# Optimization experiments

Hardware: AMD Instinct MI355X
Metric: run time of the kernel (lower is better)

Reference implementation:

```python
import jax, jax.numpy as jnp
import numpy as np

B, S, D = 4, 2048, 1024
H, DK = 16, 64
DOUT = 1024

def setup_inputs() -> dict:
    key = jax.random.key(0)
    ks = jax.random.split(key, 9)
    sc_in = 1.0 / np.sqrt(D)
    sc_cat = 1.0 / np.sqrt(H * DK)
    x = jax.random.normal(ks[0], (B, S, D), dtype=jnp.float32)
    Wq = jax.random.uniform(ks[1], (H, D, DK), jnp.float32, -sc_in, sc_in)
    bq = jax.random.uniform(ks[2], (H, DK), jnp.float32, -sc_in, sc_in)
    Wk = jax.random.uniform(ks[3], (H, D, DK), jnp.float32, -sc_in, sc_in)
    bk = jax.random.uniform(ks[4], (H, DK), jnp.float32, -sc_in, sc_in)
    Wv = jax.random.uniform(ks[5], (H, D, DK), jnp.float32, -sc_in, sc_in)
    bv = jax.random.uniform(ks[6], (H, DK), jnp.float32, -sc_in, sc_in)
    Wo = jax.random.uniform(ks[7], (H * DK, DOUT), jnp.float32, -sc_cat, sc_cat)
    bo = jax.random.uniform(ks[8], (DOUT,), jnp.float32, -sc_cat, sc_cat)
    return {"x": x, "Wq": Wq, "bq": bq, "Wk": Wk, "bk": bk, "Wv": Wv, "bv": bv, "Wo": Wo, "bo": bo}

def reference(x, Wq, bq, Wk, bk, Wv, bv, Wo, bo):
    # Per-head linear projections batched over heads: [B,S,D] x [H,D,K] -> [B,H,S,K]
    Q = jnp.einsum('bsd,hdk->bhsk', x, Wq) + bq[None, :, None, :]
    K = jnp.einsum('bsd,hdk->bhsk', x, Wk) + bk[None, :, None, :]
    V = jnp.einsum('bsd,hdk->bhsk', x, Wv) + bv[None, :, None, :]
    scale = 1.0 / jnp.sqrt(jnp.asarray(DK, dtype=x.dtype))
    scores = jnp.einsum('bhsk,bhtk->bhst', Q, K) * scale  # [B,H,S,S]
    attn = jax.nn.softmax(scores, axis=-1)
    heads = jnp.einsum('bhst,bhtk->bhsk', attn, V)  # [B,H,S,K]
    # concat heads along feature dim (head order = concat order)
    cat = jnp.transpose(heads, (0, 2, 1, 3)).reshape(x.shape[0], x.shape[1], H * DK)
    return cat @ Wo + bo
```

## Files before the change

### kernel.cpp

```cpp
#include <hip/hip_runtime.h>
#include <hip/hip_bf16.h>
#include <stdint.h>

typedef unsigned short u16;
typedef __attribute__((ext_vector_type(8))) short short8;
typedef __attribute__((ext_vector_type(4))) float f32x4;
typedef __attribute__((ext_vector_type(4))) unsigned short u16x4;

#define DEV static __device__ __forceinline__


DEV u16 f2bf(float f) {
  __hip_bfloat16 b = __float2bfloat16(f);
  return *(u16*)&b;
}

DEV void stage16(const u16* g, u16* l) {
  __builtin_amdgcn_global_load_lds((const __attribute__((address_space(1))) void*)g,
                                   (__attribute__((address_space(3))) void*)l, 16, 0, 0);
}

__global__ __launch_bounds__(256) void cvt_kernel(
    const float* __restrict__ x, const float* __restrict__ Wq,
    const float* __restrict__ Wk, const float* __restrict__ Wv,
    const float* __restrict__ Wo,
    u16* __restrict__ xb, u16* __restrict__ Wt, u16* __restrict__ Wot)
{
  int idx = blockIdx.x * 256 + threadIdx.x;
  if (idx < 1048576) {
    int i = idx * 8;
    f32x4 v0 = *(const f32x4*)&x[i];
    f32x4 v1 = *(const f32x4*)&x[i + 4];
    short8 o;
    o[0]=f2bf(v0[0]); o[1]=f2bf(v0[1]); o[2]=f2bf(v0[2]); o[3]=f2bf(v0[3]);
    o[4]=f2bf(v1[0]); o[5]=f2bf(v1[1]); o[6]=f2bf(v1[2]); o[7]=f2bf(v1[3]);
    *(short8*)&xb[i] = o;
  } else if (idx < 1835008) {
    int t = (idx - 1048576) * 4;
    int w = t >> 20; int r = t & 1048575; int n = r >> 10; int d0 = r & 1023;
    const float* W = (w == 0) ? Wq : (w == 1) ? Wk : Wv;
    int h = n >> 6, k = n & 63;
    u16x4 o;
    #pragma unroll
    for (int u = 0; u < 4; u++) o[u] = f2bf(W[(size_t)(h*1024 + d0 + u)*64 + k]);
    *(u16x4*)&Wt[t] = o;
  } else if (idx < 2097152) {
    int t = (idx - 1835008) * 4;
    int n = t >> 10, d0 = t & 1023;
    u16x4 o;
    #pragma unroll
    for (int u = 0; u < 4; u++) o[u] = f2bf(Wo[(size_t)(d0 + u)*1024 + n]);
    *(u16x4*)&Wot[t] = o;
  }
}

DEV void gemm_mainloop(const u16* __restrict__ A, const u16* __restrict__ Bt,
                       int m0, int n0, u16* As, u16* Bs, f32x4 acc[4][4])
{
  const int tid = threadIdx.x;
  const int lane = tid & 63, wid = tid >> 6;
  const int wr = wid >> 1, wc = wid & 1;
  const int qr = lane & 15, g = lane >> 4;
  const int c0 = wid * 2, rA = lane >> 2, cA = (lane & 3) * 8;

  #pragma unroll
  for (int i = 0; i < 4; i++)
    #pragma unroll
    for (int j = 0; j < 4; j++) acc[i][j] = (f32x4){0.f, 0.f, 0.f, 0.f};

  for (int kt = 0; kt < 1024; kt += 32) {
    #pragma unroll
    for (int q = 0; q < 2; q++) {
      const int c = c0 + q;
      stage16(A  + (size_t)(m0 + c*16 + rA)*1024 + kt + cA, &As[c*512]);
      stage16(Bt + (size_t)(n0 + c*16 + rA)*1024 + kt + cA, &Bs[c*512]);
    }
    __syncthreads();
    short8 af[4], bfr[4];
    #pragma unroll
    for (int i = 0; i < 4; i++) af[i]  = *(const short8*)&As[(wr*64 + i*16 + qr)*32 + g*8];
    #pragma unroll
    for (int j = 0; j < 4; j++) bfr[j] = *(const short8*)&Bs[(wc*64 + j*16 + qr)*32 + g*8];
    #pragma unroll
    for (int i = 0; i < 4; i++)
      #pragma unroll
      for (int j = 0; j < 4; j++)
        acc[i][j] = __builtin_amdgcn_mfma_f32_16x16x32_bf16(af[i], bfr[j], acc[i][j], 0, 0, 0);
    __syncthreads();
  }
}

__global__ __launch_bounds__(256) void qkv_gemm_kernel(
    const u16* __restrict__ A, const u16* __restrict__ WtAll,
    const float* __restrict__ bq, const float* __restrict__ bk, const float* __restrict__ bv,
    u16* __restrict__ Qo, u16* __restrict__ Ko, u16* __restrict__ Vo)
{
  __shared__ __align__(128) u16 As[4096];
  __shared__ __align__(128) u16 Bs[4096];
  const int lane = threadIdx.x & 63, wid = threadIdx.x >> 6;
  const int wr = wid >> 1, wc = wid & 1;
  const int qr = lane & 15, g = lane >> 4;
  const int wg = (blockIdx.x & 7) * 192 + (blockIdx.x >> 3);
  const int n0 = (wg & 7) * 128;
  const int m0 = ((wg >> 3) & 63) * 128;
  const int mode = wg >> 9;
  const u16* Bt = WtAll + (size_t)mode * 1048576;
  const float* bias = (mode == 0) ? bq : (mode == 1) ? bk : bv;
  const float osc = (mode == 0) ? 0.1803368867f : 1.0f;

  f32x4 acc[4][4];
  gemm_mainloop(A, Bt, m0, n0, As, Bs, acc);

  if (mode == 2) {
    #pragma unroll
    for (int i = 0; i < 4; i++) {
      const int mrow = m0 + wr*64 + i*16 + g*4;
      const int b = mrow >> 11, s = mrow & 2047;
      #pragma unroll
      for (int j = 0; j < 4; j++) {
        const int n = n0 + wc*64 + j*16 + qr;
        const float bz = bias[n];
        u16x4 v;
        #pragma unroll
        for (int r = 0; r < 4; r++) v[r] = f2bf(acc[i][j][r] + bz);
        *(u16x4*)&Vo[((size_t)(b*16 + (n >> 6))*64 + (n & 63))*2048 + s] = v;
      }
    }
  } else {
    u16* O = (mode == 0) ? Qo : Ko;
    #pragma unroll
    for (int i = 0; i < 4; i++) {
      const int mrow = m0 + wr*64 + i*16 + g*4;
      const int b = mrow >> 11, s = mrow & 2047;
      #pragma unroll
      for (int j = 0; j < 4; j++) {
        const int n = n0 + wc*64 + j*16 + qr;
        const float bz = bias[n];
        const size_t base = ((size_t)(b*16 + (n >> 6))*2048 + s)*64 + (n & 63);
        #pragma unroll
        for (int r = 0; r < 4; r++) O[base + (size_t)r*64] = f2bf((acc[i][j][r] + bz) * osc);
      }
    }
  }
}

__global__ __launch_bounds__(512, 2) void attn_kernel(
    const u16* __restrict__ Q, const u16* __restrict__ K,
    const u16* __restrict__ Vt, u16* __restrict__ cat)
{
  __shared__ __align__(16) u16 Ks[3][2048];
  __shared__ __align__(16) u16 Vs[3][2048];
  __shared__ __align__(16) u16 Pl[10240];
  const int lane = threadIdx.x & 63, w = threadIdx.x >> 6;
  const int bid = blockIdx.x;
  const int logical = (bid & 7) * 32 + (bid >> 3);
  const int bh = logical >> 2;
  const int xq = logical & 3;
  const int b = bh >> 4, h = bh & 15;
  const int q0 = xq * 512 + w * 64;
  const int qr = lane & 15, g = lane >> 4;
  u16* P0 = &Pl[(w*2 + 0)*640];
  u16* P1 = &Pl[(w*2 + 1)*640];

  const u16* Qb = Q  + (size_t)bh * 131072;
  const u16* Kb = K  + (size_t)bh * 131072;
  const u16* Vb = Vt + (size_t)bh * 131072;

  const int isK = (w < 4);
  const int krow = 8*w + (lane >> 3);
  const size_t ksrc = (size_t)krow*64 + (size_t)(((lane & 7) ^ (lane >> 3)) * 8);
  const int vw = w - 4, vrow = 16*vw + (lane >> 2);
  const size_t vsrc = (size_t)vrow*2048 + (size_t)(((lane & 3) ^ ((lane >> 3) & 3)) * 8);
  const int koff = w*512, voff = vw*512;

  const int kro0 = qr*64        + ((g     ^ (qr & 7)) * 8);
  const int kro1 = qr*64        + (((4+g) ^ (qr & 7)) * 8);
  const int kro2 = (16+qr)*64   + ((g     ^ (qr & 7)) * 8);
  const int kro3 = (16+qr)*64   + (((4+g) ^ (qr & 7)) * 8);
  const int vro  = qr*32        + ((g ^ ((qr >> 1) & 3)) * 8);

  short8 qa[4], qb_[4];
  #pragma unroll
  for (int qs = 0; qs < 4; qs++) {
    qa[qs]  = *(const short8*)&Qb[(size_t)(q0 + qs*16 + qr)*64 + g*8];
    qb_[qs] = *(const short8*)&Qb[(size_t)(q0 + qs*16 + qr)*64 + 32 + g*8];
  }

  const short ONE = (short)0x3F80;
  const short8 ones = {ONE, ONE, ONE, ONE, ONE, ONE, ONE, ONE};

  f32x4 o[4][4];
  #pragma unroll
  for (int qs = 0; qs < 4; qs++)
    #pragma unroll
    for (int d = 0; d < 4; d++) o[qs][d] = (f32x4){0.f,0.f,0.f,0.f};
  f32x4 ol[4] = {{0.f,0.f,0.f,0.f},{0.f,0.f,0.f,0.f},{0.f,0.f,0.f,0.f},{0.f,0.f,0.f,0.f}};

  if (isK) {
    stage16(Kb + ksrc,            &Ks[0][koff]);
    stage16(Kb + 2048 + ksrc,     &Ks[1][koff]);
  } else {
    stage16(Vb + vsrc,            &Vs[0][voff]);
    stage16(Vb + vsrc + 32,       &Vs[1][voff]);
  }

  const u16 *kc_cur = &Ks[0][0], *kc_nx1 = &Ks[1][0], *kc_stg = &Ks[2][0];
  const u16 *vc_cur = &Vs[0][0], *vc_nx1 = &Vs[1][0], *vc_stg = &Vs[2][0];

  for (int tt = 0; tt < 2048; tt += 32) {
    asm volatile("s_waitcnt vmcnt(1)" ::: "memory");
    __builtin_amdgcn_s_barrier();
    const int tn = (tt + 64) & 2047;
    if (isK) stage16(Kb + (size_t)tn*64 + ksrc, (u16*)kc_stg + koff);
    else     stage16(Vb + vsrc + tn,            (u16*)vc_stg + voff);

    short8 kc0 = *(const short8*)&kc_cur[kro0];
    short8 kc1 = *(const short8*)&kc_cur[kro1];
    short8 kc2 = *(const short8*)&kc_cur[kro2];
    short8 kc3 = *(const short8*)&kc_cur[kro3];
    short8 vv0 = *(const short8*)&vc_cur[0*512 + vro];
    short8 vv1 = *(const short8*)&vc_cur[1*512 + vro];
    short8 vv2 = *(const short8*)&vc_cur[2*512 + vro];
    short8 vv3 = *(const short8*)&vc_cur[3*512 + vro];

    #pragma unroll
    for (int qs = 0; qs < 4; qs++) {
      f32x4 sl = {0.f,0.f,0.f,0.f}, sh = {0.f,0.f,0.f,0.f};
      sl = __builtin_amdgcn_mfma_f32_16x16x32_bf16(kc0, qa[qs],  sl, 0, 0, 0);
      sl = __builtin_amdgcn_mfma_f32_16x16x32_bf16(kc1, qb_[qs], sl, 0, 0, 0);
      sh = __builtin_amdgcn_mfma_f32_16x16x32_bf16(kc2, qa[qs],  sh, 0, 0, 0);
      sh = __builtin_amdgcn_mfma_f32_16x16x32_bf16(kc3, qb_[qs], sh, 0, 0, 0);
      u16x4 lo, hi;
      #pragma unroll
      for (int r = 0; r < 4; r++) {
        lo[r] = f2bf(__builtin_amdgcn_exp2f(sl[r]));
        hi[r] = f2bf(__builtin_amdgcn_exp2f(sh[r]));
      }
      u16* P = (qs & 1) ? P1 : P0;
      *(u16x4*)&P[qr*40 + g*4]      = lo;
      *(u16x4*)&P[qr*40 + 16 + g*4] = hi;
      short8 bp = *(const short8*)&P[qr*40 + g*8];
      ol[qs] = __builtin_amdgcn_mfma_f32_16x16x32_bf16(ones, bp, ol[qs], 0, 0, 0);
      o[qs][0] = __builtin_amdgcn_mfma_f32_16x16x32_bf16(vv0, bp, o[qs][0], 0, 0, 0);
      o[qs][1] = __builtin_amdgcn_mfma_f32_16x16x32_bf16(vv1, bp, o[qs][1], 0, 0, 0);
      o[qs][2] = __builtin_amdgcn_mfma_f32_16x16x32_bf16(vv2, bp, o[qs][2], 0, 0, 0);
      o[qs][3] = __builtin_amdgcn_mfma_f32_16x16x32_bf16(vv3, bp, o[qs][3], 0, 0, 0);
    }
    const u16* t0 = kc_cur; kc_cur = kc_nx1; kc_nx1 = kc_stg; kc_stg = t0;
    const u16* t1 = vc_cur; vc_cur = vc_nx1; vc_nx1 = vc_stg; vc_stg = t1;
  }
  #pragma unroll
  for (int qs = 0; qs < 4; qs++) {
    const float inv = 1.0f / ol[qs][0];
    const size_t base = ((size_t)(b*2048 + q0 + qs*16 + qr))*1024 + h*64;
    #pragma unroll
    for (int d = 0; d < 4; d++) {
      u16x4 v;
      #pragma unroll
      for (int r = 0; r < 4; r++) v[r] = f2bf(o[qs][d][r] * inv);
      *(u16x4*)&cat[base + d*16 + g*4] = v;
    }
  }
}

__global__ __launch_bounds__(256) void out_gemm_kernel(
    const u16* __restrict__ A, const u16* __restrict__ Bt,
    const float* __restrict__ bias, float* __restrict__ out)
{
  __shared__ __align__(128) u16 As[4096];
  __shared__ __align__(128) u16 Bs[4096];
  const int lane = threadIdx.x & 63, wid = threadIdx.x >> 6;
  const int wr = wid >> 1, wc = wid & 1;
  const int qr = lane & 15, g = lane >> 4;
  const int wg = (blockIdx.x & 7) * 64 + (blockIdx.x >> 3);
  const int n0 = (wg & 7) * 128;
  const int m0 = (wg >> 3) * 128;

  f32x4 acc[4][4];
  gemm_mainloop(A, Bt, m0, n0, As, Bs, acc);

  #pragma unroll
  for (int i = 0; i < 4; i++) {
    const int mrow = m0 + wr*64 + i*16 + g*4;
    #pragma unroll
    for (int j = 0; j < 4; j++) {
      const int n = n0 + wc*64 + j*16 + qr;
      const float bz = bias[n];
      #pragma unroll
      for (int r = 0; r < 4; r++) out[(size_t)(mrow + r)*1024 + n] = acc[i][j][r] + bz;
    }
  }
}

extern "C" void kernel_launch(void* const* d_in, const int* in_sizes, int n_in,
                              void* d_out, int out_size, void* d_ws, size_t ws_size,
                              hipStream_t stream) {
  const float* x  = (const float*)d_in[0];
  const float* Wq = (const float*)d_in[1];
  const float* bq = (const float*)d_in[2];
  const float* Wk = (const float*)d_in[3];
  const float* bk = (const float*)d_in[4];
  const float* Wv = (const float*)d_in[5];
  const float* bv = (const float*)d_in[6];
  const float* Wo = (const float*)d_in[7];
  const float* bo = (const float*)d_in[8];
  float* out = (float*)d_out;
  char* ws = (char*)d_ws;

  u16* xb  = (u16*)(ws);
  u16* Wt  = (u16*)(ws + 16777216);
  u16* Wot = (u16*)(ws + 23068672);
  u16* Qb  = (u16*)(ws + 25165824);
  u16* Kb  = (u16*)(ws + 41943040);
  u16* Vt  = (u16*)(ws + 58720256);
  u16* cat = xb;

  cvt_kernel<<<8192, 256, 0, stream>>>(x, Wq, Wk, Wv, Wo, xb, Wt, Wot);
  qkv_gemm_kernel<<<1536, 256, 0, stream>>>(xb, Wt, bq, bk, bv, Qb, Kb, Vt);
  attn_kernel<<<256, 512, 0, stream>>>(Qb, Kb, Vt, cat);
  out_gemm_kernel<<<512, 256, 0, stream>>>(cat, Wot, bo, out);
}
```

Before: 195.0 us.

## Switch projection GEMMs to 256x256 tiles with double-buffered swizzled LDS pipeline

Replaces the 128x128, single-stage GEMM mainloop with a 256x256 tile computed by 8 waves. K-slices of 64 are double-buffered in LDS using XOR-swizzled layout, global-to-LDS staging is interleaved with MFMA blocks, and s_setprio is raised around the math. Both the QKV and output projection kernels use the new loop with fewer, larger workgroups. This aims to raise arithmetic intensity and hide load latency, but uses 128KB of LDS per block, which limits occupancy to one block per CU. It also leaves only 128 blocks for the output GEMM and 384 for QKV, so many CUs may sit idle or the last wave may be unbalanced.

Result: slower. 202.5 us (+3.8%).

```diff
diff --git a/kernel.cpp b/kernel.cpp
--- a/kernel.cpp
+++ b/kernel.cpp
@@ -54,67 +54,115 @@
   }
 }
 
-DEV void gemm_mainloop(const u16* __restrict__ A, const u16* __restrict__ Bt,
-                       int m0, int n0, u16* As, u16* Bs, f32x4 acc[4][4])
+
+#define RDA8(I0, BOFF) do { \
+  _Pragma("unroll") \
+  for (int i2_ = 0; i2_ < 4; i2_++) { \
+    a_[i2_][0] = *(const short8*)&As[(BOFF) + abase + (((I0)+i2_)*16 + qr)*64 + kx0]; \
+    a_[i2_][1] = *(const short8*)&As[(BOFF) + abase + (((I0)+i2_)*16 + qr)*64 + kx1]; \
+  } } while(0)
+
+#define RDB4(BV, J0, BOFF) do { \
+  _Pragma("unroll") \
+  for (int j2_ = 0; j2_ < 2; j2_++) { \
+    BV[j2_][0] = *(const short8*)&Bs[(BOFF) + bbase + (((J0)+j2_)*16 + qr)*64 + kx0]; \
+    BV[j2_][1] = *(const short8*)&Bs[(BOFF) + bbase + (((J0)+j2_)*16 + qr)*64 + kx1]; \
+  } } while(0)
+
+#define MM16(I0, J0, BV) do { \
+  __builtin_amdgcn_s_setprio(1); \
+  _Pragma("unroll") \
+  for (int i2_ = 0; i2_ < 4; i2_++) \
+    _Pragma("unroll") \
+    for (int j2_ = 0; j2_ < 2; j2_++) { \
+      acc[(I0)+i2_][(J0)+j2_] = __builtin_amdgcn_mfma_f32_16x16x32_bf16(a_[i2_][0], BV[j2_][0], acc[(I0)+i2_][(J0)+j2_], 0, 0, 0); \
+      acc[(I0)+i2_][(J0)+j2_] = __builtin_amdgcn_mfma_f32_16x16x32_bf16(a_[i2_][1], BV[j2_][1], acc[(I0)+i2_][(J0)+j2_], 0, 0, 0); \
+    } \
+  __builtin_amdgcn_s_setprio(0); } while(0)
+
+#define STGA(BUF, HALF, KOFF) do { \
+  const u16* s_ = Ax + (size_t)(m0 + (HALF)*128 + srow)*1024 + (KOFF) + schunk; \
+  stage16(s_,         &As[(BUF)*16384 + (HALF)*8192 + sdst]); \
+  stage16(s_ + 65536, &As[(BUF)*16384 + (HALF)*8192 + 4096 + sdst]); \
+} while(0)
+
+#define STGB(BUF, HALF, KOFF) do { \
+  const u16* s_ = Btp + (size_t)(n0 + (HALF)*128 + srow)*1024 + (KOFF) + schunk; \
+  stage16(s_,         &Bs[(BUF)*16384 + (HALF)*8192 + sdst]); \
+  stage16(s_ + 65536, &Bs[(BUF)*16384 + (HALF)*8192 + 4096 + sdst]); \
+} while(0)
+
+#define WBAR   do { asm volatile("s_waitcnt lgkmcnt(0)" ::: "memory"); __builtin_amdgcn_s_barrier(); } while(0)
+#define WBARV  do { asm volatile("s_waitcnt vmcnt(4) lgkmcnt(0)" ::: "memory"); __builtin_amdgcn_s_barrier(); } while(0)
+
+DEV void gemm256_mainloop(const u16* __restrict__ Ax, const u16* __restrict__ Btp,
+                          int m0, int n0, u16* As, u16* Bs, f32x4 acc[8][4])
 {
   const int tid = threadIdx.x;
-  const int lane = tid & 63, wid = tid >> 6;
-  const int wr = wid >> 1, wc = wid & 1;
-  const int qr = lane & 15, g = lane >> 4;
-  const int c0 = wid * 2, rA = lane >> 2, cA = (lane & 3) * 8;
-
-  #pragma unroll
-  for (int i = 0; i < 4; i++)
+  const int ln = tid & 63, wid = tid >> 6;
+  const int wr = wid >> 2, wc = wid & 3;
+  const int qr = ln & 15, g = ln >> 4;
+  const int srow = wid*8 + (ln >> 3);
+  const int schunk = ((ln & 7) ^ (ln >> 3)) * 8;
+  const int sdst = wid * 512;
+  const int abase = wr * 8192;
+  const int bbase = (wc >> 1) * 8192 + ((wc & 1) * 64) * 64;
+  const int kx0 = ((g    ) ^ (qr & 7)) * 8;
+  const int kx1 = ((4 + g) ^ (qr & 7)) * 8;
+
+  #pragma unroll
+  for (int i = 0; i < 8; i++)
     #pragma unroll
     for (int j = 0; j < 4; j++) acc[i][j] = (f32x4){0.f, 0.f, 0.f, 0.f};
 
-  for (int kt = 0; kt < 1024; kt += 32) {
-    #pragma unroll
-    for (int q = 0; q < 2; q++) {
-      const int c = c0 + q;
-      stage16(A  + (size_t)(m0 + c*16 + rA)*1024 + kt + cA, &As[c*512]);
-      stage16(Bt + (size_t)(n0 + c*16 + rA)*1024 + kt + cA, &Bs[c*512]);
-    }
-    __syncthreads();
-    short8 af[4], bfr[4];
-    #pragma unroll
-    for (int i = 0; i < 4; i++) af[i]  = *(const short8*)&As[(wr*64 + i*16 + qr)*32 + g*8];
-    #pragma unroll
-    for (int j = 0; j < 4; j++) bfr[j] = *(const short8*)&Bs[(wc*64 + j*16 + qr)*32 + g*8];
-    #pragma unroll
-    for (int i = 0; i < 4; i++)
-      #pragma unroll
-      for (int j = 0; j < 4; j++)
-        acc[i][j] = __builtin_amdgcn_mfma_f32_16x16x32_bf16(af[i], bfr[j], acc[i][j], 0, 0, 0);
-    __syncthreads();
-  }
-}
-
-__global__ __launch_bounds__(256) void qkv_gemm_kernel(
+  short8 a_[4][2], b01[2][2], b23[2][2];
+
+  STGB(0, 0, 0);  STGB(0, 1, 0);
+  STGA(0, 0, 0);  STGA(0, 1, 0);
+  STGB(1, 0, 64); STGB(1, 1, 64);
+  asm volatile("s_waitcnt vmcnt(4)" ::: "memory");
+  __builtin_amdgcn_s_barrier();
+
+  for (int kt = 0; kt < 1024; kt += 128) {
+    const int k1 = (kt + 64)  & 1023;
+    const int k2 = (kt + 128) & 1023;
+    const int k3 = (kt + 192) & 1023;
+    RDA8(0, 0);  RDB4(b01, 0, 0);  STGA(1, 0, k1);  WBAR;  MM16(0, 0, b01);
+    RDB4(b23, 2, 0);               STGA(1, 1, k1);  WBAR;  MM16(0, 2, b23);
+    RDA8(4, 0);                    STGB(0, 0, k2);  WBAR;  MM16(4, 0, b01);
+                                   STGB(0, 1, k2);  WBARV; MM16(4, 2, b23);
+    RDA8(0, 16384); RDB4(b01, 0, 16384); STGA(0, 0, k2); WBAR;  MM16(0, 0, b01);
+    RDB4(b23, 2, 16384);                 STGA(0, 1, k2); WBAR;  MM16(0, 2, b23);
+    RDA8(4, 16384);                      STGB(1, 0, k3); WBAR;  MM16(4, 0, b01);
+                                         STGB(1, 1, k3); WBARV; MM16(4, 2, b23);
+  }
+}
+
+__global__ __launch_bounds__(512, 2) void qkv_gemm_kernel(
     const u16* __restrict__ A, const u16* __restrict__ WtAll,
     const float* __restrict__ bq, const float* __restrict__ bk, const float* __restrict__ bv,
     u16* __restrict__ Qo, u16* __restrict__ Ko, u16* __restrict__ Vo)
 {
-  __shared__ __align__(128) u16 As[4096];
-  __shared__ __align__(128) u16 Bs[4096];
-  const int lane = threadIdx.x & 63, wid = threadIdx.x >> 6;
-  const int wr = wid >> 1, wc = wid & 1;
-  const int qr = lane & 15, g = lane >> 4;
-  const int wg = (blockIdx.x & 7) * 192 + (blockIdx.x >> 3);
-  const int n0 = (wg & 7) * 128;
-  const int m0 = ((wg >> 3) & 63) * 128;
-  const int mode = wg >> 9;
+  __shared__ __align__(16) u16 As[32768];
+  __shared__ __align__(16) u16 Bs[32768];
+  const int ln = threadIdx.x & 63, wid = threadIdx.x >> 6;
+  const int wr = wid >> 2, wc = wid & 3;
+  const int qr = ln & 15, g = ln >> 4;
+  const int wg = (blockIdx.x & 7) * 48 + (blockIdx.x >> 3);
+  const int n0 = (wg & 3) * 256;
+  const int m0 = ((wg >> 2) & 31) * 256;
+  const int mode = wg >> 7;
   const u16* Bt = WtAll + (size_t)mode * 1048576;
   const float* bias = (mode == 0) ? bq : (mode == 1) ? bk : bv;
   const float osc = (mode == 0) ? 0.1803368867f : 1.0f;
 
-  f32x4 acc[4][4];
-  gemm_mainloop(A, Bt, m0, n0, As, Bs, acc);
+  f32x4 acc[8][4];
+  gemm256_mainloop(A, Bt, m0, n0, As, Bs, acc);
 
   if (mode == 2) {
     #pragma unroll
-    for (int i = 0; i < 4; i++) {
-      const int mrow = m0 + wr*64 + i*16 + g*4;
+    for (int i = 0; i < 8; i++) {
+      const int mrow = m0 + wr*128 + i*16 + g*4;
       const int b = mrow >> 11, s = mrow & 2047;
       #pragma unroll
       for (int j = 0; j < 4; j++) {
@@ -129,8 +177,8 @@
   } else {
     u16* O = (mode == 0) ? Qo : Ko;
     #pragma unroll
-    for (int i = 0; i < 4; i++) {
-      const int mrow = m0 + wr*64 + i*16 + g*4;
+    for (int i = 0; i < 8; i++) {
+      const int mrow = m0 + wr*128 + i*16 + g*4;
       const int b = mrow >> 11, s = mrow & 2047;
       #pragma unroll
       for (int j = 0; j < 4; j++) {
@@ -197,11 +245,11 @@
   f32x4 ol[4] = {{0.f,0.f,0.f,0.f},{0.f,0.f,0.f,0.f},{0.f,0.f,0.f,0.f},{0.f,0.f,0.f,0.f}};
 
   if (isK) {
-    stage16(Kb + ksrc,            &Ks[0][koff]);
-    stage16(Kb + 2048 + ksrc,     &Ks[1][koff]);
+    stage16(Kb + ksrc,        &Ks[0][koff]);
+    stage16(Kb + 2048 + ksrc, &Ks[1][koff]);
   } else {
-    stage16(Vb + vsrc,            &Vs[0][voff]);
-    stage16(Vb + vsrc + 32,       &Vs[1][voff]);
+    stage16(Vb + vsrc,        &Vs[0][voff]);
+    stage16(Vb + vsrc + 32,   &Vs[1][voff]);
   }
 
   const u16 *kc_cur = &Ks[0][0], *kc_nx1 = &Ks[1][0], *kc_stg = &Ks[2][0];
@@ -263,25 +311,25 @@
   }
 }
 
-__global__ __launch_bounds__(256) void out_gemm_kernel(
-    const u16* __restrict__ A, const u16* __restrict__ Bt,
+__global__ __launch_bounds__(512, 2) void out_gemm_kernel(
+    const u16* __restrict__ A, const u16* __restrict__ Btp_,
     const float* __restrict__ bias, float* __restrict__ out)
 {
-  __shared__ __align__(128) u16 As[4096];
-  __shared__ __align__(128) u16 Bs[4096];
-  const int lane = threadIdx.x & 63, wid = threadIdx.x >> 6;
-  const int wr = wid >> 1, wc = wid & 1;
-  const int qr = lane & 15, g = lane >> 4;
-  const int wg = (blockIdx.x & 7) * 64 + (blockIdx.x >> 3);
-  const int n0 = (wg & 7) * 128;
-  const int m0 = (wg >> 3) * 128;
-
-  f32x4 acc[4][4];
-  gemm_mainloop(A, Bt, m0, n0, As, Bs, acc);
-
-  #pragma unroll
-  for (int i = 0; i < 4; i++) {
-    const int mrow = m0 + wr*64 + i*16 + g*4;
+  __shared__ __align__(16) u16 As[32768];
+  __shared__ __align__(16) u16 Bs[32768];
+  const int ln = threadIdx.x & 63, wid = threadIdx.x >> 6;
+  const int wr = wid >> 2, wc = wid & 3;
+  const int qr = ln & 15, g = ln >> 4;
+  const int wg = (blockIdx.x & 7) * 16 + (blockIdx.x >> 3);
+  const int n0 = (wg & 3) * 256;
+  const int m0 = (wg >> 2) * 256;
+
+  f32x4 acc[8][4];
+  gemm256_mainloop(A, Btp_, m0, n0, As, Bs, acc);
+
+  #pragma unroll
+  for (int i = 0; i < 8; i++) {
+    const int mrow = m0 + wr*128 + i*16 + g*4;
     #pragma unroll
     for (int j = 0; j < 4; j++) {
       const int n = n0 + wc*64 + j*16 + qr;
@@ -316,7 +364,7 @@
   u16* cat = xb;
 
   cvt_kernel<<<8192, 256, 0, stream>>>(x, Wq, Wk, Wv, Wo, xb, Wt, Wot);
-  qkv_gemm_kernel<<<1536, 256, 0, stream>>>(xb, Wt, bq, bk, bv, Qb, Kb, Vt);
+  qkv_gemm_kernel<<<384, 512, 0, stream>>>(xb, Wt, bq, bk, bv, Qb, Kb, Vt);
   attn_kernel<<<256, 512, 0, stream>>>(Qb, Kb, Vt, cat);
-  out_gemm_kernel<<<512, 256, 0, stream>>>(cat, Wot, bo, out);
-}
+  out_gemm_kernel<<<128, 512, 0, stream>>>(cat, Wot, bo, out);
+}
```

## Rewrite GEMM mainloop as 256x128 tile, double-buffered, XOR-swizzled LDS pipeline

Applied to the files above, without the earlier changes.

Replaces the 128x128, K=32, single-buffered GEMM mainloop used by the QKV and output projections with a 256x128 tile over 8 waves and K=64 steps. The new loop keeps two LDS stages, issues the next stage's global-to-LDS loads while MFMAs run on the current one, XOR-swizzles LDS columns to avoid bank conflicts, and raises wave priority around MFMA blocks. The aim is to hide global load latency and raise operand reuse, at the cost of much more LDS per block (96 KB) and fewer blocks in the grid.

Result: no change. 193.7 us (-0.7%).

```diff
diff --git a/kernel.cpp b/kernel.cpp
--- a/kernel.cpp
+++ b/kernel.cpp
@@ -54,62 +54,108 @@
   }
 }
 
-DEV void gemm_mainloop(const u16* __restrict__ A, const u16* __restrict__ Bt,
-                       int m0, int n0, u16* As, u16* Bs, f32x4 acc[4][4])
+
+#define RDALL(P) do { \
+  _Pragma("unroll") \
+  for (int i_ = 0; i_ < 4; i_++) { \
+    a_[i_][0] = *(const short8*)&As[(P)*16384 + (arow0 + i_*16)*64 + kx0]; \
+    a_[i_][1] = *(const short8*)&As[(P)*16384 + (arow0 + i_*16)*64 + kx1]; \
+    b_[i_][0] = *(const short8*)&Bs[(P)*8192  + (brow0 + i_*16)*64 + kx0]; \
+    b_[i_][1] = *(const short8*)&Bs[(P)*8192  + (brow0 + i_*16)*64 + kx1]; \
+  } } while(0)
+
+#define MMH(J0) do { \
+  __builtin_amdgcn_s_setprio(1); \
+  _Pragma("unroll") \
+  for (int i_ = 0; i_ < 4; i_++) \
+    _Pragma("unroll") \
+    for (int j_ = 0; j_ < 2; j_++) { \
+      acc[i_][(J0)+j_] = __builtin_amdgcn_mfma_f32_16x16x32_bf16(a_[i_][0], b_[(J0)+j_][0], acc[i_][(J0)+j_], 0, 0, 0); \
+      acc[i_][(J0)+j_] = __builtin_amdgcn_mfma_f32_16x16x32_bf16(a_[i_][1], b_[(J0)+j_][1], acc[i_][(J0)+j_], 0, 0, 0); \
+    } \
+  __builtin_amdgcn_s_setprio(0); } while(0)
+
+#define STGA(P, KK) do { \
+  _Pragma("unroll") \
+  for (int u_ = 0; u_ < 4; u_++) \
+    stage16(Ax + (size_t)(m0 + u_*64 + srow)*1024 + (KK) + schunk, \
+            &As[(P)*16384 + u_*4096 + sdst]); \
+} while(0)
+
+#define STGB(P, KK) do { \
+  _Pragma("unroll") \
+  for (int u_ = 0; u_ < 2; u_++) \
+    stage16(Btp + (size_t)(n0 + u_*64 + srow)*1024 + (KK) + schunk, \
+            &Bs[(P)*8192 + u_*4096 + sdst]); \
+} while(0)
+
+#define WB   do { asm volatile("s_waitcnt lgkmcnt(0)" ::: "memory"); __builtin_amdgcn_s_barrier(); } while(0)
+#define WBV  do { asm volatile("s_waitcnt vmcnt(6) lgkmcnt(0)" ::: "memory"); __builtin_amdgcn_s_barrier(); } while(0)
+
+DEV void gemm256x128_mainloop(const u16* __restrict__ Ax, const u16* __restrict__ Btp,
+                              int m0, int n0, u16* As, u16* Bs, f32x4 acc[4][4])
 {
   const int tid = threadIdx.x;
-  const int lane = tid & 63, wid = tid >> 6;
+  const int ln = tid & 63, wid = tid >> 6;
   const int wr = wid >> 1, wc = wid & 1;
-  const int qr = lane & 15, g = lane >> 4;
-  const int c0 = wid * 2, rA = lane >> 2, cA = (lane & 3) * 8;
+  const int qr = ln & 15, g = ln >> 4;
+  const int srow = wid*8 + (ln >> 3);
+  const int schunk = ((ln & 7) ^ (ln >> 3)) * 8;
+  const int sdst = wid * 512;
+  const int kx0 = ((g    ) ^ (qr & 7)) * 8;
+  const int kx1 = ((4 + g) ^ (qr & 7)) * 8;
+  const int arow0 = wr*64 + qr;
+  const int brow0 = wc*64 + qr;
 
   #pragma unroll
   for (int i = 0; i < 4; i++)
     #pragma unroll
     for (int j = 0; j < 4; j++) acc[i][j] = (f32x4){0.f, 0.f, 0.f, 0.f};
 
-  for (int kt = 0; kt < 1024; kt += 32) {
-    #pragma unroll
-    for (int q = 0; q < 2; q++) {
-      const int c = c0 + q;
-      stage16(A  + (size_t)(m0 + c*16 + rA)*1024 + kt + cA, &As[c*512]);
-      stage16(Bt + (size_t)(n0 + c*16 + rA)*1024 + kt + cA, &Bs[c*512]);
-    }
-    __syncthreads();
-    short8 af[4], bfr[4];
-    #pragma unroll
-    for (int i = 0; i < 4; i++) af[i]  = *(const short8*)&As[(wr*64 + i*16 + qr)*32 + g*8];
-    #pragma unroll
-    for (int j = 0; j < 4; j++) bfr[j] = *(const short8*)&Bs[(wc*64 + j*16 + qr)*32 + g*8];
-    #pragma unroll
-    for (int i = 0; i < 4; i++)
-      #pragma unroll
-      for (int j = 0; j < 4; j++)
-        acc[i][j] = __builtin_amdgcn_mfma_f32_16x16x32_bf16(af[i], bfr[j], acc[i][j], 0, 0, 0);
-    __syncthreads();
-  }
-}
-
-__global__ __launch_bounds__(256) void qkv_gemm_kernel(
+  short8 a_[4][2], b_[4][2];
+
+  STGA(0, 0);  STGB(0, 0);
+  STGA(1, 64); STGB(1, 64);
+  asm volatile("s_waitcnt vmcnt(6)" ::: "memory");
+  __builtin_amdgcn_s_barrier();
+
+  for (int t = 0; t < 16; t += 2) {
+    RDALL(0);
+    WB;
+    MMH(0);
+    { const int k2 = ((t + 2) & 15) * 64; STGA(0, k2); STGB(0, k2); }
+    WBV;
+    MMH(2);
+    RDALL(1);
+    WB;
+    MMH(0);
+    { const int k3 = ((t + 3) & 15) * 64; STGA(1, k3); STGB(1, k3); }
+    WBV;
+    MMH(2);
+  }
+}
+
+__global__ __launch_bounds__(512, 2) void qkv_gemm_kernel(
     const u16* __restrict__ A, const u16* __restrict__ WtAll,
     const float* __restrict__ bq, const float* __restrict__ bk, const float* __restrict__ bv,
     u16* __restrict__ Qo, u16* __restrict__ Ko, u16* __restrict__ Vo)
 {
-  __shared__ __align__(128) u16 As[4096];
-  __shared__ __align__(128) u16 Bs[4096];
-  const int lane = threadIdx.x & 63, wid = threadIdx.x >> 6;
+  __shared__ __align__(16) u16 As[32768];
+  __shared__ __align__(16) u16 Bs[16384];
+  const int ln = threadIdx.x & 63, wid = threadIdx.x >> 6;
   const int wr = wid >> 1, wc = wid & 1;
-  const int qr = lane & 15, g = lane >> 4;
-  const int wg = (blockIdx.x & 7) * 192 + (blockIdx.x >> 3);
-  const int n0 = (wg & 7) * 128;
-  const int m0 = ((wg >> 3) & 63) * 128;
-  const int mode = wg >> 9;
-  const u16* Bt = WtAll + (size_t)mode * 1048576;
+  const int qr = ln & 15, g = ln >> 4;
+  const int wg = (blockIdx.x & 7) * 96 + (blockIdx.x >> 3);
+  const int mode = wg >> 8;
+  const int rem = wg & 255;
+  const int n0 = (rem & 7) * 128;
+  const int m0 = (rem >> 3) * 256;
+  const u16* Btp = WtAll + (size_t)mode * 1048576;
   const float* bias = (mode == 0) ? bq : (mode == 1) ? bk : bv;
   const float osc = (mode == 0) ? 0.1803368867f : 1.0f;
 
   f32x4 acc[4][4];
-  gemm_mainloop(A, Bt, m0, n0, As, Bs, acc);
+  gemm256x128_mainloop(A, Btp, m0, n0, As, Bs, acc);
 
   if (mode == 2) {
     #pragma unroll
@@ -197,11 +243,11 @@
   f32x4 ol[4] = {{0.f,0.f,0.f,0.f},{0.f,0.f,0.f,0.f},{0.f,0.f,0.f,0.f},{0.f,0.f,0.f,0.f}};
 
   if (isK) {
-    stage16(Kb + ksrc,            &Ks[0][koff]);
-    stage16(Kb + 2048 + ksrc,     &Ks[1][koff]);
+    stage16(Kb + ksrc,        &Ks[0][koff]);
+    stage16(Kb + 2048 + ksrc, &Ks[1][koff]);
   } else {
-    stage16(Vb + vsrc,            &Vs[0][voff]);
-    stage16(Vb + vsrc + 32,       &Vs[1][voff]);
+    stage16(Vb + vsrc,        &Vs[0][voff]);
+    stage16(Vb + vsrc + 32,   &Vs[1][voff]);
   }
 
   const u16 *kc_cur = &Ks[0][0], *kc_nx1 = &Ks[1][0], *kc_stg = &Ks[2][0];
@@ -263,21 +309,21 @@
   }
 }
 
-__global__ __launch_bounds__(256) void out_gemm_kernel(
-    const u16* __restrict__ A, const u16* __restrict__ Bt,
+__global__ __launch_bounds__(512, 2) void out_gemm_kernel(
+    const u16* __restrict__ A, const u16* __restrict__ Btp_,
     const float* __restrict__ bias, float* __restrict__ out)
 {
-  __shared__ __align__(128) u16 As[4096];
-  __shared__ __align__(128) u16 Bs[4096];
-  const int lane = threadIdx.x & 63, wid = threadIdx.x >> 6;
+  __shared__ __align__(16) u16 As[32768];
+  __shared__ __align__(16) u16 Bs[16384];
+  const int ln = threadIdx.x & 63, wid = threadIdx.x >> 6;
   const int wr = wid >> 1, wc = wid & 1;
-  const int qr = lane & 15, g = lane >> 4;
-  const int wg = (blockIdx.x & 7) * 64 + (blockIdx.x >> 3);
+  const int qr = ln & 15, g = ln >> 4;
+  const int wg = (blockIdx.x & 7) * 32 + (blockIdx.x >> 3);
   const int n0 = (wg & 7) * 128;
-  const int m0 = (wg >> 3) * 128;
+  const int m0 = (wg >> 3) * 256;
 
   f32x4 acc[4][4];
-  gemm_mainloop(A, Bt, m0, n0, As, Bs, acc);
+  gemm256x128_mainloop(A, Btp_, m0, n0, As, Bs, acc);
 
   #pragma unroll
   for (int i = 0; i < 4; i++) {
@@ -316,7 +362,7 @@
   u16* cat = xb;
 
   cvt_kernel<<<8192, 256, 0, stream>>>(x, Wq, Wk, Wv, Wo, xb, Wt, Wot);
-  qkv_gemm_kernel<<<1536, 256, 0, stream>>>(xb, Wt, bq, bk, bv, Qb, Kb, Vt);
+  qkv_gemm_kernel<<<768, 512, 0, stream>>>(xb, Wt, bq, bk, bv, Qb, Kb, Vt);
   attn_kernel<<<256, 512, 0, stream>>>(Qb, Kb, Vt, cat);
-  out_gemm_kernel<<<512, 256, 0, stream>>>(cat, Wot, bo, out);
-}
+  out_gemm_kernel<<<256, 512, 0, stream>>>(cat, Wot, bo, out);
+}
```
